# Optimization experiments

Hardware: AMD Instinct MI355X
Metric: run time of the kernel (lower is better)

The kernel has to match this reference:

```python
import jax, jax.numpy as jnp
import numpy as np

N_NODES = 5000
N_EDGES = 40000
NUM_ATOM_TYPES = 100
HID = 32            # multiplicity of 0e and 1o in irreps_hidden
EDGE_ATTR_DIM = 8
NUM_BOND_TYPES = 5
OUT_SCALARS = 2 * 6 + 1  # max_charge=6 -> 13x0e
CUTOFF = 5.0
SQRT3 = 1.7320508075688772


def _sh(edge_vec):
    # o3.SphericalHarmonics('1x0e + 1x1o', normalize=True, normalization='component')
    d = jnp.sqrt(jnp.sum(edge_vec * edge_vec, axis=-1) + 1e-12)
    n = edge_vec / d[:, None]
    sh0 = jnp.ones(edge_vec.shape[0], edge_vec.dtype)          # [E]
    sh1 = SQRT3 * n[:, (1, 2, 0)]                              # [E,3], e3nn (y,z,x) order
    return sh0, sh1, d


def _soft_one_hot(d):
    # e3nn.math.soft_one_hot_linspace(d, 0, cutoff, 8, basis='gaussian', cutoff=True)
    values = jnp.linspace(0.0, CUTOFF, EDGE_ATTR_DIM + 2)[1:-1]
    step = CUTOFF / (EDGE_ATTR_DIM + 1)
    diff = (d[:, None] - values[None, :]) / step
    return jnp.exp(-diff * diff) / 1.12


def _mlp(x, W0, b0, W1, b1):
    # ScalarMLP(in, out, hidden=[in], SiLU)
    return jax.nn.silu(x @ W0 + b0) @ W1 + b1


def _tp_init(s, sh0, sh1, w):
    # FCTP(32x0e, 1x0e+1x1o -> 32x0e+32x1o); paths: 0e*0e->0e, 0e*1o->1o
    E = s.shape[0]
    w1 = w[:, : HID * HID].reshape(E, HID, HID)
    w2 = w[:, HID * HID :].reshape(E, HID, HID)
    c = 1.0 / np.sqrt(HID)  # fan-in = 32 per output irrep
    out_s = c * jnp.einsum('eu,euw->ew', s * sh0[:, None], w1)
    out_v = c * jnp.einsum('eu,ei,euw->ewi', s, sh1, w2)
    return out_s, out_v


def _tp_hidden(s, v, sh0, sh1, w):
    # FCTP(32x0e+32x1o, 1x0e+1x1o -> 32x0e+32x1o)
    # path order: 0e*0e->0e, 0e*1o->1o, 1o*0e->1o, 1o*1o->0e
    E = s.shape[0]
    ws = w.reshape(E, 4, HID, HID)
    c = 1.0 / np.sqrt(2 * HID)  # fan-in = 64 per output irrep
    dot = jnp.einsum('eui,ei->eu', v, sh1) / SQRT3  # CG(1,1->0) = delta/sqrt(3)
    out_s = c * (jnp.einsum('eu,euw->ew', s * sh0[:, None], ws[:, 0]) +
                 jnp.einsum('eu,euw->ew', dot, ws[:, 3]))
    out_v = c * (jnp.einsum('eu,ei,euw->ewi', s, sh1, ws[:, 1]) +
                 jnp.einsum('eui,euw->ewi', v * sh0[:, None, None], ws[:, 2]))
    return out_s, out_v


def _edge_tp(s1, v1, s2, v2, sh0, sh1, w):
    # FCTP(64x0e+64x1o (concat of two hidden), 1x0e+1x1o -> 5x0e)
    # blocks in concat order: s_src, v_src, s_dst, v_dst
    E = s1.shape[0]
    ws = w.reshape(E, 4, HID, NUM_BOND_TYPES)
    c = 1.0 / np.sqrt(4 * HID)  # fan-in = 128
    d1 = jnp.einsum('eui,ei->eu', v1, sh1) / SQRT3
    d2 = jnp.einsum('eui,ei->eu', v2, sh1) / SQRT3
    return c * (jnp.einsum('eu,euw->ew', s1 * sh0[:, None], ws[:, 0]) +
                jnp.einsum('eu,euw->ew', d1, ws[:, 1]) +
                jnp.einsum('eu,euw->ew', s2 * sh0[:, None], ws[:, 2]) +
                jnp.einsum('eu,euw->ew', d2, ws[:, 3]))


def _scatter_mean(ms, mv, dst, n):
    cnt = jax.ops.segment_sum(jnp.ones(dst.shape[0], ms.dtype), dst, num_segments=n)
    cnt = jnp.maximum(cnt, 1.0)
    s = jax.ops.segment_sum(ms, dst, num_segments=n) / cnt[:, None]
    v = jax.ops.segment_sum(mv, dst, num_segments=n) / cnt[:, None, None]
    return s, v


def setup_inputs() -> dict:
    key = jax.random.key(0)
    ks = jax.random.split(key, 16)
    def w(k, shape, fan_in):
        return jax.random.normal(k, shape, dtype=jnp.float32) / np.sqrt(fan_in)
    inp = {}
    inp['coordinates'] = jax.random.normal(ks[0], (N_NODES, 3), dtype=jnp.float32) * 1.5
    inp['atom_types'] = jax.random.randint(ks[1], (N_NODES,), 0, NUM_ATOM_TYPES)
    inp['edge_index'] = jax.random.randint(ks[2], (2, N_EDGES), 0, N_NODES)
    inp['atom_embed'] = jax.random.normal(ks[3], (NUM_ATOM_TYPES, HID), dtype=jnp.float32)
    inp['ip_W0'] = w(ks[4], (EDGE_ATTR_DIM, EDGE_ATTR_DIM), EDGE_ATTR_DIM)
    inp['ip_b0'] = jnp.zeros((EDGE_ATTR_DIM,), jnp.float32)
    inp['ip_W1'] = w(ks[5], (EDGE_ATTR_DIM, 2 * HID * HID), EDGE_ATTR_DIM)
    inp['ip_b1'] = jnp.zeros((2 * HID * HID,), jnp.float32)
    inp['ly_W0'] = w(ks[6], (EDGE_ATTR_DIM, EDGE_ATTR_DIM), EDGE_ATTR_DIM)
    inp['ly_b0'] = jnp.zeros((EDGE_ATTR_DIM,), jnp.float32)
    inp['ly_W1'] = w(ks[7], (EDGE_ATTR_DIM, 4 * HID * HID), EDGE_ATTR_DIM)
    inp['ly_b1'] = jnp.zeros((4 * HID * HID,), jnp.float32)
    inp['ly_Ws'] = jax.random.normal(ks[8], (HID, HID), dtype=jnp.float32)
    inp['ly_Wv'] = jax.random.normal(ks[9], (HID, HID), dtype=jnp.float32)
    inp['et_W0'] = w(ks[10], (EDGE_ATTR_DIM, EDGE_ATTR_DIM), EDGE_ATTR_DIM)
    inp['et_b0'] = jnp.zeros((EDGE_ATTR_DIM,), jnp.float32)
    inp['et_W1'] = w(ks[11], (EDGE_ATTR_DIM, 4 * HID * NUM_BOND_TYPES), EDGE_ATTR_DIM)
    inp['et_b1'] = jnp.zeros((4 * HID * NUM_BOND_TYPES,), jnp.float32)
    inp['no_W1'] = jax.random.normal(ks[12], (HID, OUT_SCALARS), dtype=jnp.float32)
    inp['no_W2'] = jax.random.normal(ks[13], (OUT_SCALARS, OUT_SCALARS), dtype=jnp.float32)
    return inp


def reference(coordinates, atom_types, edge_index, atom_embed,
              ip_W0, ip_b0, ip_W1, ip_b1,
              ly_W0, ly_b0, ly_W1, ly_b1, ly_Ws, ly_Wv,
              et_W0, et_b0, et_W1, et_b1, no_W1, no_W2):
    n = coordinates.shape[0]
    src, dst = edge_index[0], edge_index[1]
    edge_vec = coordinates[dst] - coordinates[src]
    sh0, sh1, d = _sh(edge_vec)
    edge_attr = _soft_one_hot(d)                              # [E,8]
    # initial projector: Conv(32x0e -> 32x0e+32x1o)
    s0 = atom_embed[atom_types]                               # [N,32]
    w_ip = _mlp(edge_attr, ip_W0, ip_b0, ip_W1, ip_b1)        # [E,2048]
    ms, mv = _tp_init(s0[src], sh0, sh1, w_ip)
    s, v = _scatter_mean(ms, mv, dst, n)                      # [N,32],[N,32,3]
    # one LinearSelfInteraction(Conv) layer
    w_ly = _mlp(edge_attr, ly_W0, ly_b0, ly_W1, ly_b1)        # [E,4096]
    ms, mv = _tp_hidden(s[src], v[src], sh0, sh1, w_ly)
    cs, cv = _scatter_mean(ms, mv, dst, n)
    lc = 1.0 / np.sqrt(HID)  # e3nn o3.Linear normalization
    s = cs + lc * (s @ ly_Ws)
    v = cv + lc * jnp.einsum('eui,uw->ewi', v, ly_Wv)
    # edge output: FCTP([h_src, h_dst], edge_sh) with radial weights
    w_et = _mlp(edge_attr, et_W0, et_b0, et_W1, et_b1)        # [E,640]
    edge_out = _edge_tp(s[src], v[src], s[dst], v[dst], sh0, sh1, w_et)  # [E,5]
    # node output MLP on detached scalar channel (13x0e)
    sd = jax.lax.stop_gradient(s)
    h = jax.nn.silu(sd @ no_W1 / np.sqrt(HID))
    node_out = h @ no_W2 / np.sqrt(OUT_SCALARS)               # [N,13]
    return edge_out, node_out
```

## Files before the change

kernel.cpp:

```cpp
#include <hip/hip_runtime.h>

#define NN 5000
#define NE 40000
#define HB 320

typedef unsigned int u32;
typedef unsigned short u16;
typedef __fp16 h16x2 __attribute__((ext_vector_type(2)));
typedef _Float16 f16x8 __attribute__((ext_vector_type(8)));
typedef __attribute__((ext_vector_type(4))) float f32x4;

union AF { u32 u[4]; f16x8 v; uint4 q; };

__device__ __forceinline__ float siluf(float x) { return x / (1.f + __expf(-x)); }

__device__ __forceinline__ u32 f2bf_u(float f) {
  u32 x = __float_as_uint(f);
  return (x + 0x7FFFu + ((x >> 16) & 1u)) >> 16;
}
__device__ __forceinline__ u16 f2bf(float f) { return (u16)f2bf_u(f); }
__device__ __forceinline__ float bf2f(u16 v) { return __uint_as_float(((u32)v) << 16); }
__device__ __forceinline__ u32 packbf2(float lo, float hi) {
  return f2bf_u(lo) | (f2bf_u(hi) << 16);
}
__device__ __forceinline__ u32 pkh2(float a, float b) {
  union { h16x2 h; u32 u; } r;
  r.h = __builtin_amdgcn_cvt_pkrtz(a, b);
  return r.u;
}
__device__ __forceinline__ u16 f2h(float v) {
  _Float16 h = (_Float16)v;
  return *(u16*)&h;
}
__device__ __forceinline__ void unpack8(uint4 q, float* f) {
  f[0] = __uint_as_float(q.x << 16); f[1] = __uint_as_float(q.x & 0xFFFF0000u);
  f[2] = __uint_as_float(q.y << 16); f[3] = __uint_as_float(q.y & 0xFFFF0000u);
  f[4] = __uint_as_float(q.z << 16); f[5] = __uint_as_float(q.z & 0xFFFF0000u);
  f[6] = __uint_as_float(q.w << 16); f[7] = __uint_as_float(q.w & 0xFFFF0000u);
}
__device__ __forceinline__ float dot8f(const float* h, const float* w, float init) {
  float a = init;
#pragma unroll
  for (int k = 0; k < 8; k++) a = fmaf(h[k], w[k], a);
  return a;
}
__device__ __forceinline__ void mlp8(const float* ea, const float* __restrict__ W0,
                                     const float* __restrict__ b0, float* h) {
#pragma unroll
  for (int j = 0; j < 8; j++) {
    float a = b0[j];
#pragma unroll
    for (int i = 0; i < 8; i++) a += ea[i] * W0[i*8 + j];
    h[j] = siluf(a);
  }
}
__device__ __forceinline__ AF mkfrag(float hs, const float* s) {
  AF a;
  a.u[0] = pkh2(hs*s[0], hs*s[1]);
  a.u[1] = pkh2(hs*s[2], hs*s[3]);
  a.u[2] = pkh2(hs*s[4], hs*s[5]);
  a.u[3] = pkh2(hs*s[6], hs*s[7]);
  return a;
}

__global__ __launch_bounds__(256) void k_conv1g(
    const float* __restrict__ coords, const int* __restrict__ eidx,
    const float* __restrict__ emb, const int* __restrict__ atype,
    const float* __restrict__ ipW0, const float* __restrict__ ipb0,
    const float* __restrict__ lyW0, const float* __restrict__ lyb0,
    const float* __restrict__ etW0, const float* __restrict__ etb0,
    const float* __restrict__ W1, const float* __restrict__ b1,
    const float* __restrict__ lyW1, const float* __restrict__ lyb1,
    float* __restrict__ sh, float* __restrict__ h_ip,
    float* __restrict__ h_ly, float* __restrict__ h_et,
    int* __restrict__ cur, int* __restrict__ perm,
    u16* __restrict__ msg, u16* __restrict__ lyT) {
  if (blockIdx.x >= HB) {
    int b = blockIdx.x - HB;
    int h = b >> 3;
    int t0 = (b & 7)*2304 + threadIdx.x*9;
#pragma unroll
    for (int j = 0; j < 9; j++) {
      int t = t0 + j;
      int kch = t >> 9, rem = t & 511;
      int col = rem >> 3, kk = rem & 7;
      int k = kch*8 + kk;
      int basec = (h == 0) ? ((col >> 5)*1024 + (col & 31))
                           : ((col < 32) ? (2048 + col) : (3072 + (col - 32)));
      float v = (k < 256) ? lyW1[(k >> 5)*4096 + basec + (k & 31)*32]
                          : lyb1[basec + (k - 256)*32];
      lyT[h*18432 + t] = f2h(v);
    }
    return;
  }
  __shared__ __align__(16) u16 B2[36*64*8];
  {
    int col = threadIdx.x & 63, pth = col >> 5, w = col & 31;
    int k0 = (threadIdx.x >> 6) * 72;
    for (int k = k0; k < k0 + 72; k++) {
      float v = (k < 256) ? W1[(k >> 5)*2048 + pth*1024 + (k & 31)*32 + w]
                          : b1[pth*1024 + (k - 256)*32 + w];
      B2[((k >> 3)*64 + col)*8 + (k & 7)] = f2h(v);
    }
  }
  if (threadIdx.x < 128) {
    int idx = threadIdx.x;
    int w = (idx >> 4) & 3, j = idx >> 6, m = idx & 15;
    int tile = blockIdx.x*4 + w + j*(HB*4);
    if (tile*16 < NE) {
      int e = tile*16 + m;
      int s = eidx[e], d = eidx[NE + e];
      float vx = coords[d*3+0] - coords[s*3+0];
      float vy = coords[d*3+1] - coords[s*3+1];
      float vz = coords[d*3+2] - coords[s*3+2];
      float dist = sqrtf(vx*vx + vy*vy + vz*vz + 1e-12f);
      float inv = 1.f / dist;
      const float SQ3 = 1.7320508075688772f;
      sh[e*3+0] = SQ3 * vy * inv;
      sh[e*3+1] = SQ3 * vz * inv;
      sh[e*3+2] = SQ3 * vx * inv;
      float ea[8];
      const float step = 5.f / 9.f;
#pragma unroll
      for (int jj = 0; jj < 8; jj++) {
        float diff = (dist - step * (float)(jj+1)) * (9.f / 5.f);
        ea[jj] = __expf(-diff*diff) * (1.f / 1.12f);
      }
      float h[8];
      mlp8(ea, ipW0, ipb0, h);
#pragma unroll
      for (int jj = 0; jj < 8; jj++) h_ip[e*8+jj] = h[jj];
      mlp8(ea, lyW0, lyb0, h);
#pragma unroll
      for (int jj = 0; jj < 8; jj++) h_ly[e*8+jj] = h[jj];
      mlp8(ea, etW0, etb0, h);
#pragma unroll
      for (int jj = 0; jj < 8; jj++) h_et[e*8+jj] = h[jj];
      int* cp = &cur[d];
      atomicCAS(cp, (int)0xAAAAAAAA, 0);
      int t = atomicAdd(cp, 1);
      if (t < 64) perm[d*64 + t] = e;
    }
  }
  __syncthreads();
  int lane = threadIdx.x & 63;
  int m = lane & 15, q = lane >> 4, wid = threadIdx.x >> 6;
  const float cs = 0.17677669529663687f;
  for (int tile = blockIdx.x*4 + wid; tile*16 < NE; tile += HB*4) {
    int e = tile*16 + m;
    int srow = atype[eidx[e]];
    float4 sA = *(const float4*)&emb[srow*32 + q*8];
    float4 sB = *(const float4*)&emb[srow*32 + q*8 + 4];
    float4 hA = *(const float4*)&h_ip[e*8];
    float4 hB = *(const float4*)&h_ip[e*8 + 4];
    float sf[8] = {sA.x,sA.y,sA.z,sA.w,sB.x,sB.y,sB.z,sB.w};
    float hf[8] = {hA.x,hA.y,hA.z,hA.w,hB.x,hB.y,hB.z,hB.w};
    f32x4 acc0 = {0.f,0.f,0.f,0.f}, acc1 = acc0, acc2 = acc0, acc3 = acc0;
#pragma unroll
    for (int ks = 0; ks < 9; ks++) {
      float hs = (ks < 8) ? hf[ks] : 1.f;
      AF a = mkfrag(hs, sf);
      int c2 = (ks*4 + q)*64;
      AF b0, b1f, b2, b3;
      b0.q  = *(const uint4*)&B2[(c2 +  0 + m)*8];
      b1f.q = *(const uint4*)&B2[(c2 + 16 + m)*8];
      b2.q  = *(const uint4*)&B2[(c2 + 32 + m)*8];
      b3.q  = *(const uint4*)&B2[(c2 + 48 + m)*8];
      acc0 = __builtin_amdgcn_mfma_f32_16x16x32_f16(a.v, b0.v,  acc0, 0, 0, 0);
      acc1 = __builtin_amdgcn_mfma_f32_16x16x32_f16(a.v, b1f.v, acc1, 0, 0, 0);
      acc2 = __builtin_amdgcn_mfma_f32_16x16x32_f16(a.v, b2.v,  acc2, 0, 0, 0);
      acc3 = __builtin_amdgcn_mfma_f32_16x16x32_f16(a.v, b3.v,  acc3, 0, 0, 0);
    }
#pragma unroll
    for (int r = 0; r < 4; r++) {
      int et = tile*16 + q*4 + r;
      u16* mp = msg + (size_t)et*128;
      mp[m]      = f2bf(cs*acc0[r]);
      mp[16 + m] = f2bf(cs*acc1[r]);
      float s0v = sh[et*3+0], s1v = sh[et*3+1], s2v = sh[et*3+2];
      float m0 = cs*acc2[r], m1 = cs*acc3[r];
      mp[32 +      m] = f2bf(m0*s0v);
      mp[64 +      m] = f2bf(m0*s1v);
      mp[96 +      m] = f2bf(m0*s2v);
      mp[32 + 16 + m] = f2bf(m1*s0v);
      mp[64 + 16 + m] = f2bf(m1*s1v);
      mp[96 + 16 + m] = f2bf(m1*s2v);
    }
  }
}

__global__ __launch_bounds__(256) void k_conv2(
    const float* __restrict__ hE, const float* __restrict__ sh,
    const float* __restrict__ s1, const float* __restrict__ v1soa,
    const int* __restrict__ eidx, const u16* __restrict__ lyT,
    u16* __restrict__ msgA, u16* __restrict__ msgB) {
  __shared__ __align__(16) u16 B2[36*64*8];
  const bool scalarHalf = blockIdx.x < HB;
  int blk = scalarHalf ? blockIdx.x : blockIdx.x - HB;
  {
    const uint4* src4 = (const uint4*)(lyT + (scalarHalf ? 0 : 18432));
    uint4* dst4 = (uint4*)B2;
    for (int t = threadIdx.x; t < 2304; t += 256) dst4[t] = src4[t];
  }
  __syncthreads();
  int lane = threadIdx.x & 63;
  int m = lane & 15, q = lane >> 4, wid = threadIdx.x >> 6;
  const float c = 0.125f;
  for (int tile = blk*4 + wid; tile*16 < NE; tile += HB*4) {
    int e = tile*16 + m;
    int srcn = eidx[e];
    float4 hA = *(const float4*)&hE[e*8];
    float4 hB = *(const float4*)&hE[e*8 + 4];
    float hf[8] = {hA.x,hA.y,hA.z,hA.w,hB.x,hB.y,hB.z,hB.w};

    if (scalarHalf) {
      float4 sA = *(const float4*)&s1[srcn*32 + q*8];
      float4 sB = *(const float4*)&s1[srcn*32 + q*8 + 4];
      float sf[8] = {sA.x,sA.y,sA.z,sA.w,sB.x,sB.y,sB.z,sB.w};
      f32x4 acc0 = {0.f,0.f,0.f,0.f}, acc1 = acc0, acc2 = acc0, acc3 = acc0;
#pragma unroll
      for (int ks = 0; ks < 9; ks++) {
        float hs = (ks < 8) ? hf[ks] : 1.f;
        AF a = mkfrag(hs, sf);
        int c2 = (ks*4 + q)*64;
        AF b0, b1f, b2, b3;
        b0.q  = *(const uint4*)&B2[(c2 +  0 + m)*8];
        b1f.q = *(const uint4*)&B2[(c2 + 16 + m)*8];
        b2.q  = *(const uint4*)&B2[(c2 + 32 + m)*8];
        b3.q  = *(const uint4*)&B2[(c2 + 48 + m)*8];
        acc0 = __builtin_amdgcn_mfma_f32_16x16x32_f16(a.v, b0.v,  acc0, 0, 0, 0);
        acc1 = __builtin_amdgcn_mfma_f32_16x16x32_f16(a.v, b1f.v, acc1, 0, 0, 0);
        acc2 = __builtin_amdgcn_mfma_f32_16x16x32_f16(a.v, b2.v,  acc2, 0, 0, 0);
        acc3 = __builtin_amdgcn_mfma_f32_16x16x32_f16(a.v, b3.v,  acc3, 0, 0, 0);
      }
#pragma unroll
      for (int r = 0; r < 4; r++) {
        int et = tile*16 + q*4 + r;
        u16* mp = msgA + (size_t)et*128;
        mp[m]      = f2bf(c*acc0[r]);
        mp[16 + m] = f2bf(c*acc1[r]);
        float s0v = sh[et*3+0], s1v = sh[et*3+1], s2v = sh[et*3+2];
        float m0 = c*acc2[r], m1 = c*acc3[r];
        mp[32 +      m] = f2bf(m0*s0v);
        mp[64 +      m] = f2bf(m0*s1v);
        mp[96 +      m] = f2bf(m0*s2v);
        mp[32 + 16 + m] = f2bf(m1*s0v);
        mp[64 + 16 + m] = f2bf(m1*s1v);
        mp[96 + 16 + m] = f2bf(m1*s2v);
      }
    } else {
      const float is3 = 0.5773502691896258f;
      float vf[3][8];
#pragma unroll
      for (int i = 0; i < 3; i++) {
        float4 aa = *(const float4*)&v1soa[i*160000 + srcn*32 + q*8];
        float4 bb = *(const float4*)&v1soa[i*160000 + srcn*32 + q*8 + 4];
        vf[i][0]=aa.x; vf[i][1]=aa.y; vf[i][2]=aa.z; vf[i][3]=aa.w;
        vf[i][4]=bb.x; vf[i][5]=bb.y; vf[i][6]=bb.z; vf[i][7]=bb.w;
      }
      float es0 = sh[e*3+0], es1 = sh[e*3+1], es2 = sh[e*3+2];
      float df[8];
#pragma unroll
      for (int j = 0; j < 8; j++)
        df[j] = (vf[0][j]*es0 + vf[1][j]*es1 + vf[2][j]*es2) * is3;
      f32x4 z = {0.f,0.f,0.f,0.f};
      f32x4 aV00 = z, aV01 = z, aV10 = z, aV11 = z, aV20 = z, aV21 = z, aD0 = z, aD1 = z;
#pragma unroll
      for (int ks = 0; ks < 9; ks++) {
        float hs = (ks < 8) ? hf[ks] : 1.f;
        int c2 = (ks*4 + q)*64;
        AF b0, b1f, b2, b3;
        b0.q  = *(const uint4*)&B2[(c2 +  0 + m)*8];
        b1f.q = *(const uint4*)&B2[(c2 + 16 + m)*8];
        b2.q  = *(const uint4*)&B2[(c2 + 32 + m)*8];
        b3.q  = *(const uint4*)&B2[(c2 + 48 + m)*8];
        AF a0 = mkfrag(hs, vf[0]);
        AF a1 = mkfrag(hs, vf[1]);
        AF a2 = mkfrag(hs, vf[2]);
        AF ad = mkfrag(hs, df);
        aV00 = __builtin_amdgcn_mfma_f32_16x16x32_f16(a0.v, b0.v,  aV00, 0, 0, 0);
        aV01 = __builtin_amdgcn_mfma_f32_16x16x32_f16(a0.v, b1f.v, aV01, 0, 0, 0);
        aV10 = __builtin_amdgcn_mfma_f32_16x16x32_f16(a1.v, b0.v,  aV10, 0, 0, 0);
        aV11 = __builtin_amdgcn_mfma_f32_16x16x32_f16(a1.v, b1f.v, aV11, 0, 0, 0);
        aV20 = __builtin_amdgcn_mfma_f32_16x16x32_f16(a2.v, b0.v,  aV20, 0, 0, 0);
        aV21 = __builtin_amdgcn_mfma_f32_16x16x32_f16(a2.v, b1f.v, aV21, 0, 0, 0);
        aD0  = __builtin_amdgcn_mfma_f32_16x16x32_f16(ad.v, b2.v,  aD0,  0, 0, 0);
        aD1  = __builtin_amdgcn_mfma_f32_16x16x32_f16(ad.v, b3.v,  aD1,  0, 0, 0);
      }
#pragma unroll
      for (int r = 0; r < 4; r++) {
        int et = tile*16 + q*4 + r;
        u16* mp = msgB + (size_t)et*128;
        mp[m]      = f2bf(c*aD0[r]);
        mp[16 + m] = f2bf(c*aD1[r]);
        mp[32 +      m] = f2bf(c*aV00[r]);
        mp[32 + 16 + m] = f2bf(c*aV01[r]);
        mp[64 +      m] = f2bf(c*aV10[r]);
        mp[64 + 16 + m] = f2bf(c*aV11[r]);
        mp[96 +      m] = f2bf(c*aV20[r]);
        mp[96 + 16 + m] = f2bf(c*aV21[r]);
      }
    }
  }
}

__global__ __launch_bounds__(256) void k_gather1(
    const u16* __restrict__ msg, const int* __restrict__ perm,
    const int* __restrict__ cur, float* __restrict__ s1,
    float* __restrict__ v1soa) {
  __shared__ int pe[2][64];
  int ln = threadIdx.x >> 7, c = threadIdx.x & 127;
  int n = blockIdx.x*2 + ln;
  int deg = min(cur[n], 64);
  if (c < 64) pe[ln][c] = perm[n*64 + c];
  __syncthreads();
  float acc = 0.f;
  for (int j = 0; j < deg; j++)
    acc += bf2f(msg[(size_t)pe[ln][j]*128 + c]);
  acc /= (float)max(deg, 1);
  if (c < 32) s1[n*32 + c] = acc;
  else { int i = (c-32) >> 5, w = (c-32) & 31; v1soa[i*160000 + n*32 + w] = acc; }
}

__global__ __launch_bounds__(256) void k_gather2(
    const u16* __restrict__ msgA, const u16* __restrict__ msgB,
    const int* __restrict__ perm, const int* __restrict__ cur,
    const float* __restrict__ s1, const float* __restrict__ v1soa,
    const float* __restrict__ Ws, const float* __restrict__ Wv,
    const float* __restrict__ noW1, const float* __restrict__ noW2,
    float* __restrict__ s2, float* __restrict__ v2, float* __restrict__ outN) {
  __shared__ int pe[2][64];
  __shared__ float sb[2][32];
  __shared__ float hb[2][13];
  int ln = threadIdx.x >> 7, c = threadIdx.x & 127;
  int n = blockIdx.x*2 + ln;
  int deg = min(cur[n], 64);
  if (c < 64) pe[ln][c] = perm[n*64 + c];
  __syncthreads();
  float acc = 0.f;
  for (int j = 0; j < deg; j++) {
    int e = pe[ln][j];
    acc += bf2f(msgA[(size_t)e*128 + c]) + bf2f(msgB[(size_t)e*128 + c]);
  }
  acc /= (float)max(deg, 1);
  const float lc = 0.17677669529663687f;
  if (c < 32) {
    float ss = 0.f;
#pragma unroll 8
    for (int u = 0; u < 32; u++) ss += s1[n*32 + u] * Ws[u*32 + c];
    float val = acc + lc*ss;
    s2[n*32 + c] = val;
    sb[ln][c] = val;
  } else {
    int i = (c-32) >> 5, w = (c-32) & 31;
    float sv = 0.f;
#pragma unroll 8
    for (int u = 0; u < 32; u++) sv += v1soa[i*160000 + n*32 + u] * Wv[u*32 + w];
    v2[n*96 + w*3 + i] = acc + lc*sv;
  }
  __syncthreads();
  const float i32 = 0.17677669529663687f;
  if (c < 13) {
    float a = 0.f;
#pragma unroll 8
    for (int u = 0; u < 32; u++) a += sb[ln][u] * noW1[u*13 + c];
    hb[ln][c] = siluf(a * i32);
  }
  __syncthreads();
  const float i13 = 0.2773500981126146f;
  if (c < 13) {
    float a = 0.f;
#pragma unroll
    for (int j = 0; j < 13; j++) a += hb[ln][j] * noW2[j*13 + c];
    outN[n*13 + c] = a * i13;
  }
}

__global__ __launch_bounds__(256) void k_e3(
    const float* __restrict__ hE, const float* __restrict__ sh,
    const float* __restrict__ s2, const float* __restrict__ v2,
    const int* __restrict__ eidx,
    const float* __restrict__ W1, const float* __restrict__ b1,
    float* __restrict__ out) {
  __shared__ uint4 WQ[640];
  __shared__ float BQ[640];
  for (int t = threadIdx.x; t < 640; t += 256) {
    int u = t & 31, pw = t >> 5, p2 = pw / 5, w = pw - p2*5;
    int col = p2*160 + u*5 + w;
    const float* s = W1 + col;
    uint4 q;
    q.x = packbf2(s[0],      s[640]);
    q.y = packbf2(s[1280],   s[1920]);
    q.z = packbf2(s[2560],   s[3200]);
    q.w = packbf2(s[3840],   s[4480]);
    WQ[t] = q;
    BQ[t] = b1[col];
  }
  __syncthreads();
  const int g = threadIdx.x >> 5, tw = threadIdx.x & 31;
  const float c = 0.08838834764831845f;
  const float is3 = 0.5773502691896258f;
  for (int p = blockIdx.x*8 + g; p*2 < NE; p += gridDim.x*8) {
    int e0 = p*2, e1 = e0 + 1;
    float h0[8], h1[8];
    {
      float4 qa = *(const float4*)&hE[e0*8];
      float4 qb = *(const float4*)&hE[e0*8+4];
      h0[0]=qa.x; h0[1]=qa.y; h0[2]=qa.z; h0[3]=qa.w;
      h0[4]=qb.x; h0[5]=qb.y; h0[6]=qb.z; h0[7]=qb.w;
      float4 qc = *(const float4*)&hE[e1*8];
      float4 qd = *(const float4*)&hE[e1*8+4];
      h1[0]=qc.x; h1[1]=qc.y; h1[2]=qc.z; h1[3]=qc.w;
      h1[4]=qd.x; h1[5]=qd.y; h1[6]=qd.z; h1[7]=qd.w;
    }
    int sA = eidx[e0], dA = eidx[NE+e0];
    int sB = eidx[e1], dB = eidx[NE+e1];
    float sa0 = sh[e0*3+0], sa1 = sh[e0*3+1], sa2 = sh[e0*3+2];
    float sb0 = sh[e1*3+0], sb1 = sh[e1*3+1], sb2 = sh[e1*3+2];
    float c00 = s2[sA*32 + tw];
    float c01 = (v2[sA*96+tw*3+0]*sa0 + v2[sA*96+tw*3+1]*sa1 + v2[sA*96+tw*3+2]*sa2) * is3;
    float c02 = s2[dA*32 + tw];
    float c03 = (v2[dA*96+tw*3+0]*sa0 + v2[dA*96+tw*3+1]*sa1 + v2[dA*96+tw*3+2]*sa2) * is3;
    float c10 = s2[sB*32 + tw];
    float c11 = (v2[sB*96+tw*3+0]*sb0 + v2[sB*96+tw*3+1]*sb1 + v2[sB*96+tw*3+2]*sb2) * is3;
    float c12 = s2[dB*32 + tw];
    float c13 = (v2[dB*96+tw*3+0]*sb0 + v2[dB*96+tw*3+1]*sb1 + v2[dB*96+tw*3+2]*sb2) * is3;
    float part0[5] = {0,0,0,0,0};
    float part1[5] = {0,0,0,0,0};
#pragma unroll
    for (int pp = 0; pp < 4; pp++) {
      float cp0 = (pp==0) ? c00 : (pp==1) ? c01 : (pp==2) ? c02 : c03;
      float cp1 = (pp==0) ? c10 : (pp==1) ? c11 : (pp==2) ? c12 : c13;
#pragma unroll
      for (int w = 0; w < 5; w++) {
        int idx = (pp*5 + w)*32 + tw;
        float f[8];
        unpack8(WQ[idx], f);
        float bv = BQ[idx];
        part0[w] = fmaf(cp0, dot8f(h0, f, bv), part0[w]);
        part1[w] = fmaf(cp1, dot8f(h1, f, bv), part1[w]);
      }
    }
#pragma unroll
    for (int off = 16; off > 0; off >>= 1)
#pragma unroll
      for (int w = 0; w < 5; w++) {
        part0[w] += __shfl_xor(part0[w], off, 32);
        part1[w] += __shfl_xor(part1[w], off, 32);
      }
    float outv = 0.f;
#pragma unroll
    for (int w = 0; w < 5; w++) {
      if (tw == w)     outv = part0[w];
      if (tw == 5 + w) outv = part1[w];
    }
    if (tw < 10) out[e0*5 + tw] = c * outv;
  }
}

extern "C" void kernel_launch(void* const* d_in, const int* in_sizes, int n_in,
                              void* d_out, int out_size, void* d_ws, size_t ws_size,
                              hipStream_t stream) {
  (void)in_sizes; (void)n_in; (void)out_size; (void)ws_size;
  const float* coords = (const float*)d_in[0];
  const int*   atype  = (const int*)d_in[1];
  const int*   eidx   = (const int*)d_in[2];
  const float* emb    = (const float*)d_in[3];
  const float* ipW0 = (const float*)d_in[4];
  const float* ipb0 = (const float*)d_in[5];
  const float* ipW1 = (const float*)d_in[6];
  const float* ipb1 = (const float*)d_in[7];
  const float* lyW0 = (const float*)d_in[8];
  const float* lyb0 = (const float*)d_in[9];
  const float* lyW1 = (const float*)d_in[10];
  const float* lyb1 = (const float*)d_in[11];
  const float* lyWs = (const float*)d_in[12];
  const float* lyWv = (const float*)d_in[13];
  const float* etW0 = (const float*)d_in[14];
  const float* etb0 = (const float*)d_in[15];
  const float* etW1 = (const float*)d_in[16];
  const float* etb1 = (const float*)d_in[17];
  const float* noW1 = (const float*)d_in[18];
  const float* noW2 = (const float*)d_in[19];

  float* ws = (float*)d_ws;
  float* sh    = ws;
  float* h_ip  = ws + 120000;
  float* h_ly  = ws + 440000;
  float* h_et  = ws + 760000;
  float* s1    = ws + 1240000;
  float* v1soa = ws + 1400000;
  float* s2    = ws + 1880000;
  float* v2    = ws + 2040000;
  int*   cur   = (int*)(ws + 2520000);
  int*   perm  = (int*)(ws + 2525000);
  u16*   msgA  = (u16*)(ws + 2845000);
  u16*   msgB  = (u16*)(ws + 5405000);
  u16*   lyT   = (u16*)(ws + 7965000);

  float* outE = (float*)d_out;
  float* outN = (float*)d_out + NE*5;

  k_conv1g<<<HB + 16, 256, 0, stream>>>(coords, eidx, emb, atype,
                                        ipW0, ipb0, lyW0, lyb0, etW0, etb0,
                                        ipW1, ipb1, lyW1, lyb1,
                                        sh, h_ip, h_ly, h_et, cur, perm, msgA, lyT);
  k_gather1<<<NN/2, 256, 0, stream>>>(msgA, perm, cur, s1, v1soa);
  k_conv2<<<2*HB, 256, 0, stream>>>(h_ly, sh, s1, v1soa, eidx, lyT, msgA, msgB);
  k_gather2<<<NN/2, 256, 0, stream>>>(msgA, msgB, perm, cur, s1, v1soa,
                                      lyWs, lyWv, noW1, noW2, s2, v2, outN);
  k_e3<<<1024, 256, 0, stream>>>(h_et, sh, s2, v2, eidx, etW1, etb1, outE);
}
```

Measured before the change: 170.0 us.

## Fuse all five stage kernels into one cooperative persistent kernel with grid syncs

Replaces the five separate launches (conv1, gather1, conv2, gather2, edge output) with one cooperative kernel that moves between stages using grid.sync. The goal is to remove the launch gaps and tail effects between the small kernels. The grid size is capped by occupancy and MAXGRID, so each stage now runs as a grid-stride loop over fewer blocks than the original per-kernel launch sizes. The gathers are also reworked to give one wavefront per node, reading the per-node edge list through shuffles. The costs are grid-barrier overhead, less parallelism in the stages that previously used large grids, and a tighter register budget under launch_bounds(256,2).

```diff
diff --git a/kernel.cpp b/kernel.cpp
--- a/kernel.cpp
+++ b/kernel.cpp
@@ -1,8 +1,11 @@
 #include <hip/hip_runtime.h>
+#include <hip/hip_cooperative_groups.h>
+
+namespace cg = cooperative_groups;
 
 #define NN 5000
 #define NE 40000
-#define HB 320
+#define MAXGRID 512
 
 typedef unsigned int u32;
 typedef unsigned short u16;
@@ -63,22 +66,38 @@
   return a;
 }
 
-__global__ __launch_bounds__(256) void k_conv1g(
-    const float* __restrict__ coords, const int* __restrict__ eidx,
-    const float* __restrict__ emb, const int* __restrict__ atype,
-    const float* __restrict__ ipW0, const float* __restrict__ ipb0,
-    const float* __restrict__ lyW0, const float* __restrict__ lyb0,
-    const float* __restrict__ etW0, const float* __restrict__ etb0,
-    const float* __restrict__ W1, const float* __restrict__ b1,
-    const float* __restrict__ lyW1, const float* __restrict__ lyb1,
-    float* __restrict__ sh, float* __restrict__ h_ip,
-    float* __restrict__ h_ly, float* __restrict__ h_et,
-    int* __restrict__ cur, int* __restrict__ perm,
-    u16* __restrict__ msg, u16* __restrict__ lyT) {
-  if (blockIdx.x >= HB) {
-    int b = blockIdx.x - HB;
+struct Par {
+  const float* coords; const int* atype; const int* eidx; const float* emb;
+  const float* ipW0; const float* ipb0; const float* ipW1; const float* ipb1;
+  const float* lyW0; const float* lyb0; const float* lyW1; const float* lyb1;
+  const float* lyWs; const float* lyWv;
+  const float* etW0; const float* etb0; const float* etW1; const float* etb1;
+  const float* noW1; const float* noW2;
+  float* sh; float* h_ip; float* h_ly; float* h_et;
+  float* s1; float* v1soa; float* s2; float* v2;
+  int* cur; int* perm; u16* msgA; u16* msgB; u16* lyT;
+  float* outE; float* outN;
+};
+
+union SMem {
+  u16 B2[18432];
+  struct { uint4 WQ[640]; float BQ[640]; } e;
+};
+
+__global__ __launch_bounds__(256, 2) void k_all(Par par) {
+  __shared__ SMem sm;
+  cg::grid_group grid = cg::this_grid();
+  const int tid = threadIdx.x;
+  const int bid = blockIdx.x;
+  const int lane = tid & 63;
+  const int m = lane & 15, q = lane >> 4, wid = tid >> 6;
+  const int ngrid = (int)gridDim.x;
+  const int ncb = ngrid - 16;
+
+  if (bid >= ncb) {
+    int b = bid - ncb;
     int h = b >> 3;
-    int t0 = (b & 7)*2304 + threadIdx.x*9;
+    int t0 = (b & 7)*2304 + tid*9;
 #pragma unroll
     for (int j = 0; j < 9; j++) {
       int t = t0 + j;
@@ -87,136 +106,70 @@
       int k = kch*8 + kk;
       int basec = (h == 0) ? ((col >> 5)*1024 + (col & 31))
                            : ((col < 32) ? (2048 + col) : (3072 + (col - 32)));
-      float v = (k < 256) ? lyW1[(k >> 5)*4096 + basec + (k & 31)*32]
-                          : lyb1[basec + (k - 256)*32];
-      lyT[h*18432 + t] = f2h(v);
-    }
-    return;
-  }
-  __shared__ __align__(16) u16 B2[36*64*8];
-  {
-    int col = threadIdx.x & 63, pth = col >> 5, w = col & 31;
-    int k0 = (threadIdx.x >> 6) * 72;
-    for (int k = k0; k < k0 + 72; k++) {
-      float v = (k < 256) ? W1[(k >> 5)*2048 + pth*1024 + (k & 31)*32 + w]
-                          : b1[pth*1024 + (k - 256)*32 + w];
-      B2[((k >> 3)*64 + col)*8 + (k & 7)] = f2h(v);
-    }
-  }
-  if (threadIdx.x < 128) {
-    int idx = threadIdx.x;
-    int w = (idx >> 4) & 3, j = idx >> 6, m = idx & 15;
-    int tile = blockIdx.x*4 + w + j*(HB*4);
-    if (tile*16 < NE) {
+      float v = (k < 256) ? par.lyW1[(k >> 5)*4096 + basec + (k & 31)*32]
+                          : par.lyb1[basec + (k - 256)*32];
+      par.lyT[h*18432 + t] = f2h(v);
+    }
+  } else {
+    {
+      int col = tid & 63, pth = col >> 5, w = col & 31;
+      int k0 = (tid >> 6) * 72;
+      for (int k = k0; k < k0 + 72; k++) {
+        float v = (k < 256) ? par.ipW1[(k >> 5)*2048 + pth*1024 + (k & 31)*32 + w]
+                            : par.ipb1[pth*1024 + (k - 256)*32 + w];
+        sm.B2[((k >> 3)*64 + col)*8 + (k & 7)] = f2h(v);
+      }
+    }
+    if (tid < 128) {
+      int w = (tid >> 4) & 3, mm = tid & 15, jj0 = tid >> 6;
+      for (int it = jj0; ; it += 2) {
+        int tile = bid*4 + w + it*(ncb*4);
+        if (tile*16 >= NE) break;
+        int e = tile*16 + mm;
+        int s = par.eidx[e], d = par.eidx[NE + e];
+        float vx = par.coords[d*3+0] - par.coords[s*3+0];
+        float vy = par.coords[d*3+1] - par.coords[s*3+1];
+        float vz = par.coords[d*3+2] - par.coords[s*3+2];
+        float dist = sqrtf(vx*vx + vy*vy + vz*vz + 1e-12f);
+        float inv = 1.f / dist;
+        const float SQ3 = 1.7320508075688772f;
+        par.sh[e*3+0] = SQ3 * vy * inv;
+        par.sh[e*3+1] = SQ3 * vz * inv;
+        par.sh[e*3+2] = SQ3 * vx * inv;
+        float ea[8];
+        const float step = 5.f / 9.f;
+#pragma unroll
+        for (int jj = 0; jj < 8; jj++) {
+          float diff = (dist - step * (float)(jj+1)) * (9.f / 5.f);
+          ea[jj] = __expf(-diff*diff) * (1.f / 1.12f);
+        }
+        float h[8];
+        mlp8(ea, par.ipW0, par.ipb0, h);
+#pragma unroll
+        for (int jj = 0; jj < 8; jj++) par.h_ip[e*8+jj] = h[jj];
+        mlp8(ea, par.lyW0, par.lyb0, h);
+#pragma unroll
+        for (int jj = 0; jj < 8; jj++) par.h_ly[e*8+jj] = h[jj];
+        mlp8(ea, par.etW0, par.etb0, h);
+#pragma unroll
+        for (int jj = 0; jj < 8; jj++) par.h_et[e*8+jj] = h[jj];
+        int* cp = &par.cur[d];
+        atomicCAS(cp, (int)0xAAAAAAAA, 0);
+        int t = atomicAdd(cp, 1);
+        if (t < 64) par.perm[d*64 + t] = e;
+      }
+    }
+    __syncthreads();
+    const float cs = 0.17677669529663687f;
+    for (int tile = bid*4 + wid; tile*16 < NE; tile += ncb*4) {
       int e = tile*16 + m;
-      int s = eidx[e], d = eidx[NE + e];
-      float vx = coords[d*3+0] - coords[s*3+0];
-      float vy = coords[d*3+1] - coords[s*3+1];
-      float vz = coords[d*3+2] - coords[s*3+2];
-      float dist = sqrtf(vx*vx + vy*vy + vz*vz + 1e-12f);
-      float inv = 1.f / dist;
-      const float SQ3 = 1.7320508075688772f;
-      sh[e*3+0] = SQ3 * vy * inv;
-      sh[e*3+1] = SQ3 * vz * inv;
-      sh[e*3+2] = SQ3 * vx * inv;
-      float ea[8];
-      const float step = 5.f / 9.f;
-#pragma unroll
-      for (int jj = 0; jj < 8; jj++) {
-        float diff = (dist - step * (float)(jj+1)) * (9.f / 5.f);
-        ea[jj] = __expf(-diff*diff) * (1.f / 1.12f);
-      }
-      float h[8];
-      mlp8(ea, ipW0, ipb0, h);
-#pragma unroll
-      for (int jj = 0; jj < 8; jj++) h_ip[e*8+jj] = h[jj];
-      mlp8(ea, lyW0, lyb0, h);
-#pragma unroll
-      for (int jj = 0; jj < 8; jj++) h_ly[e*8+jj] = h[jj];
-      mlp8(ea, etW0, etb0, h);
-#pragma unroll
-      for (int jj = 0; jj < 8; jj++) h_et[e*8+jj] = h[jj];
-      int* cp = &cur[d];
-      atomicCAS(cp, (int)0xAAAAAAAA, 0);
-      int t = atomicAdd(cp, 1);
-      if (t < 64) perm[d*64 + t] = e;
-    }
-  }
-  __syncthreads();
-  int lane = threadIdx.x & 63;
-  int m = lane & 15, q = lane >> 4, wid = threadIdx.x >> 6;
-  const float cs = 0.17677669529663687f;
-  for (int tile = blockIdx.x*4 + wid; tile*16 < NE; tile += HB*4) {
-    int e = tile*16 + m;
-    int srow = atype[eidx[e]];
-    float4 sA = *(const float4*)&emb[srow*32 + q*8];
-    float4 sB = *(const float4*)&emb[srow*32 + q*8 + 4];
-    float4 hA = *(const float4*)&h_ip[e*8];
-    float4 hB = *(const float4*)&h_ip[e*8 + 4];
-    float sf[8] = {sA.x,sA.y,sA.z,sA.w,sB.x,sB.y,sB.z,sB.w};
-    float hf[8] = {hA.x,hA.y,hA.z,hA.w,hB.x,hB.y,hB.z,hB.w};
-    f32x4 acc0 = {0.f,0.f,0.f,0.f}, acc1 = acc0, acc2 = acc0, acc3 = acc0;
-#pragma unroll
-    for (int ks = 0; ks < 9; ks++) {
-      float hs = (ks < 8) ? hf[ks] : 1.f;
-      AF a = mkfrag(hs, sf);
-      int c2 = (ks*4 + q)*64;
-      AF b0, b1f, b2, b3;
-      b0.q  = *(const uint4*)&B2[(c2 +  0 + m)*8];
-      b1f.q = *(const uint4*)&B2[(c2 + 16 + m)*8];
-      b2.q  = *(const uint4*)&B2[(c2 + 32 + m)*8];
-      b3.q  = *(const uint4*)&B2[(c2 + 48 + m)*8];
-      acc0 = __builtin_amdgcn_mfma_f32_16x16x32_f16(a.v, b0.v,  acc0, 0, 0, 0);
-      acc1 = __builtin_amdgcn_mfma_f32_16x16x32_f16(a.v, b1f.v, acc1, 0, 0, 0);
-      acc2 = __builtin_amdgcn_mfma_f32_16x16x32_f16(a.v, b2.v,  acc2, 0, 0, 0);
-      acc3 = __builtin_amdgcn_mfma_f32_16x16x32_f16(a.v, b3.v,  acc3, 0, 0, 0);
-    }
-#pragma unroll
-    for (int r = 0; r < 4; r++) {
-      int et = tile*16 + q*4 + r;
-      u16* mp = msg + (size_t)et*128;
-      mp[m]      = f2bf(cs*acc0[r]);
-      mp[16 + m] = f2bf(cs*acc1[r]);
-      float s0v = sh[et*3+0], s1v = sh[et*3+1], s2v = sh[et*3+2];
-      float m0 = cs*acc2[r], m1 = cs*acc3[r];
-      mp[32 +      m] = f2bf(m0*s0v);
-      mp[64 +      m] = f2bf(m0*s1v);
-      mp[96 +      m] = f2bf(m0*s2v);
-      mp[32 + 16 + m] = f2bf(m1*s0v);
-      mp[64 + 16 + m] = f2bf(m1*s1v);
-      mp[96 + 16 + m] = f2bf(m1*s2v);
-    }
-  }
-}
-
-__global__ __launch_bounds__(256) void k_conv2(
-    const float* __restrict__ hE, const float* __restrict__ sh,
-    const float* __restrict__ s1, const float* __restrict__ v1soa,
-    const int* __restrict__ eidx, const u16* __restrict__ lyT,
-    u16* __restrict__ msgA, u16* __restrict__ msgB) {
-  __shared__ __align__(16) u16 B2[36*64*8];
-  const bool scalarHalf = blockIdx.x < HB;
-  int blk = scalarHalf ? blockIdx.x : blockIdx.x - HB;
-  {
-    const uint4* src4 = (const uint4*)(lyT + (scalarHalf ? 0 : 18432));
-    uint4* dst4 = (uint4*)B2;
-    for (int t = threadIdx.x; t < 2304; t += 256) dst4[t] = src4[t];
-  }
-  __syncthreads();
-  int lane = threadIdx.x & 63;
-  int m = lane & 15, q = lane >> 4, wid = threadIdx.x >> 6;
-  const float c = 0.125f;
-  for (int tile = blk*4 + wid; tile*16 < NE; tile += HB*4) {
-    int e = tile*16 + m;
-    int srcn = eidx[e];
-    float4 hA = *(const float4*)&hE[e*8];
-    float4 hB = *(const float4*)&hE[e*8 + 4];
-    float hf[8] = {hA.x,hA.y,hA.z,hA.w,hB.x,hB.y,hB.z,hB.w};
-
-    if (scalarHalf) {
-      float4 sA = *(const float4*)&s1[srcn*32 + q*8];
-      float4 sB = *(const float4*)&s1[srcn*32 + q*8 + 4];
+      int srow = par.atype[par.eidx[e]];
+      float4 sA = *(const float4*)&par.emb[srow*32 + q*8];
+      float4 sB = *(const float4*)&par.emb[srow*32 + q*8 + 4];
+      float4 hA = *(const float4*)&par.h_ip[e*8];
+      float4 hB = *(const float4*)&par.h_ip[e*8 + 4];
       float sf[8] = {sA.x,sA.y,sA.z,sA.w,sB.x,sB.y,sB.z,sB.w};
+      float hf[8] = {hA.x,hA.y,hA.z,hA.w,hB.x,hB.y,hB.z,hB.w};
       f32x4 acc0 = {0.f,0.f,0.f,0.f}, acc1 = acc0, acc2 = acc0, acc3 = acc0;
 #pragma unroll
       for (int ks = 0; ks < 9; ks++) {
@@ -224,10 +177,10 @@
         AF a = mkfrag(hs, sf);
         int c2 = (ks*4 + q)*64;
         AF b0, b1f, b2, b3;
-        b0.q  = *(const uint4*)&B2[(c2 +  0 + m)*8];
-        b1f.q = *(const uint4*)&B2[(c2 + 16 + m)*8];
-        b2.q  = *(const uint4*)&B2[(c2 + 32 + m)*8];
-        b3.q  = *(const uint4*)&B2[(c2 + 48 + m)*8];
+        b0.q  = *(const uint4*)&sm.B2[(c2 +  0 + m)*8];
+        b1f.q = *(const uint4*)&sm.B2[(c2 + 16 + m)*8];
+        b2.q  = *(const uint4*)&sm.B2[(c2 + 32 + m)*8];
+        b3.q  = *(const uint4*)&sm.B2[(c2 + 48 + m)*8];
         acc0 = __builtin_amdgcn_mfma_f32_16x16x32_f16(a.v, b0.v,  acc0, 0, 0, 0);
         acc1 = __builtin_amdgcn_mfma_f32_16x16x32_f16(a.v, b1f.v, acc1, 0, 0, 0);
         acc2 = __builtin_amdgcn_mfma_f32_16x16x32_f16(a.v, b2.v,  acc2, 0, 0, 0);
@@ -236,11 +189,11 @@
 #pragma unroll
       for (int r = 0; r < 4; r++) {
         int et = tile*16 + q*4 + r;
-        u16* mp = msgA + (size_t)et*128;
-        mp[m]      = f2bf(c*acc0[r]);
-        mp[16 + m] = f2bf(c*acc1[r]);
-        float s0v = sh[et*3+0], s1v = sh[et*3+1], s2v = sh[et*3+2];
-        float m0 = c*acc2[r], m1 = c*acc3[r];
+        u16* mp = par.msgA + (size_t)et*128;
+        mp[m]      = f2bf(cs*acc0[r]);
+        mp[16 + m] = f2bf(cs*acc1[r]);
+        float s0v = par.sh[et*3+0], s1v = par.sh[et*3+1], s2v = par.sh[et*3+2];
+        float m0 = cs*acc2[r], m1 = cs*acc3[r];
         mp[32 +      m] = f2bf(m0*s0v);
         mp[64 +      m] = f2bf(m0*s1v);
         mp[96 +      m] = f2bf(m0*s2v);
@@ -248,213 +201,268 @@
         mp[64 + 16 + m] = f2bf(m1*s1v);
         mp[96 + 16 + m] = f2bf(m1*s2v);
       }
-    } else {
-      const float is3 = 0.5773502691896258f;
-      float vf[3][8];
-#pragma unroll
-      for (int i = 0; i < 3; i++) {
-        float4 aa = *(const float4*)&v1soa[i*160000 + srcn*32 + q*8];
-        float4 bb = *(const float4*)&v1soa[i*160000 + srcn*32 + q*8 + 4];
-        vf[i][0]=aa.x; vf[i][1]=aa.y; vf[i][2]=aa.z; vf[i][3]=aa.w;
-        vf[i][4]=bb.x; vf[i][5]=bb.y; vf[i][6]=bb.z; vf[i][7]=bb.w;
-      }
-      float es0 = sh[e*3+0], es1 = sh[e*3+1], es2 = sh[e*3+2];
-      float df[8];
-#pragma unroll
-      for (int j = 0; j < 8; j++)
-        df[j] = (vf[0][j]*es0 + vf[1][j]*es1 + vf[2][j]*es2) * is3;
-      f32x4 z = {0.f,0.f,0.f,0.f};
-      f32x4 aV00 = z, aV01 = z, aV10 = z, aV11 = z, aV20 = z, aV21 = z, aD0 = z, aD1 = z;
-#pragma unroll
-      for (int ks = 0; ks < 9; ks++) {
-        float hs = (ks < 8) ? hf[ks] : 1.f;
-        int c2 = (ks*4 + q)*64;
-        AF b0, b1f, b2, b3;
-        b0.q  = *(const uint4*)&B2[(c2 +  0 + m)*8];
-        b1f.q = *(const uint4*)&B2[(c2 + 16 + m)*8];
-        b2.q  = *(const uint4*)&B2[(c2 + 32 + m)*8];
-        b3.q  = *(const uint4*)&B2[(c2 + 48 + m)*8];
-        AF a0 = mkfrag(hs, vf[0]);
-        AF a1 = mkfrag(hs, vf[1]);
-        AF a2 = mkfrag(hs, vf[2]);
-        AF ad = mkfrag(hs, df);
-        aV00 = __builtin_amdgcn_mfma_f32_16x16x32_f16(a0.v, b0.v,  aV00, 0, 0, 0);
-        aV01 = __builtin_amdgcn_mfma_f32_16x16x32_f16(a0.v, b1f.v, aV01, 0, 0, 0);
-        aV10 = __builtin_amdgcn_mfma_f32_16x16x32_f16(a1.v, b0.v,  aV10, 0, 0, 0);
-        aV11 = __builtin_amdgcn_mfma_f32_16x16x32_f16(a1.v, b1f.v, aV11, 0, 0, 0);
-        aV20 = __builtin_amdgcn_mfma_f32_16x16x32_f16(a2.v, b0.v,  aV20, 0, 0, 0);
-        aV21 = __builtin_amdgcn_mfma_f32_16x16x32_f16(a2.v, b1f.v, aV21, 0, 0, 0);
-        aD0  = __builtin_amdgcn_mfma_f32_16x16x32_f16(ad.v, b2.v,  aD0,  0, 0, 0);
-        aD1  = __builtin_amdgcn_mfma_f32_16x16x32_f16(ad.v, b3.v,  aD1,  0, 0, 0);
-      }
-#pragma unroll
-      for (int r = 0; r < 4; r++) {
-        int et = tile*16 + q*4 + r;
-        u16* mp = msgB + (size_t)et*128;
-        mp[m]      = f2bf(c*aD0[r]);
-        mp[16 + m] = f2bf(c*aD1[r]);
-        mp[32 +      m] = f2bf(c*aV00[r]);
-        mp[32 + 16 + m] = f2bf(c*aV01[r]);
-        mp[64 +      m] = f2bf(c*aV10[r]);
-        mp[64 + 16 + m] = f2bf(c*aV11[r]);
-        mp[96 +      m] = f2bf(c*aV20[r]);
-        mp[96 + 16 + m] = f2bf(c*aV21[r]);
-      }
-    }
-  }
-}
-
-__global__ __launch_bounds__(256) void k_gather1(
-    const u16* __restrict__ msg, const int* __restrict__ perm,
-    const int* __restrict__ cur, float* __restrict__ s1,
-    float* __restrict__ v1soa) {
-  __shared__ int pe[2][64];
-  int ln = threadIdx.x >> 7, c = threadIdx.x & 127;
-  int n = blockIdx.x*2 + ln;
-  int deg = min(cur[n], 64);
-  if (c < 64) pe[ln][c] = perm[n*64 + c];
-  __syncthreads();
-  float acc = 0.f;
-  for (int j = 0; j < deg; j++)
-    acc += bf2f(msg[(size_t)pe[ln][j]*128 + c]);
-  acc /= (float)max(deg, 1);
-  if (c < 32) s1[n*32 + c] = acc;
-  else { int i = (c-32) >> 5, w = (c-32) & 31; v1soa[i*160000 + n*32 + w] = acc; }
-}
-
-__global__ __launch_bounds__(256) void k_gather2(
-    const u16* __restrict__ msgA, const u16* __restrict__ msgB,
-    const int* __restrict__ perm, const int* __restrict__ cur,
-    const float* __restrict__ s1, const float* __restrict__ v1soa,
-    const float* __restrict__ Ws, const float* __restrict__ Wv,
-    const float* __restrict__ noW1, const float* __restrict__ noW2,
-    float* __restrict__ s2, float* __restrict__ v2, float* __restrict__ outN) {
-  __shared__ int pe[2][64];
-  __shared__ float sb[2][32];
-  __shared__ float hb[2][13];
-  int ln = threadIdx.x >> 7, c = threadIdx.x & 127;
-  int n = blockIdx.x*2 + ln;
-  int deg = min(cur[n], 64);
-  if (c < 64) pe[ln][c] = perm[n*64 + c];
-  __syncthreads();
-  float acc = 0.f;
-  for (int j = 0; j < deg; j++) {
-    int e = pe[ln][j];
-    acc += bf2f(msgA[(size_t)e*128 + c]) + bf2f(msgB[(size_t)e*128 + c]);
-  }
-  acc /= (float)max(deg, 1);
-  const float lc = 0.17677669529663687f;
-  if (c < 32) {
-    float ss = 0.f;
+    }
+  }
+  __threadfence();
+  grid.sync();
+
+  {
+    int wg = (bid << 2) | wid;
+    for (int n = wg; n < NN; n += ngrid*4) {
+      int deg = min(par.cur[n], 64);
+      int pv = par.perm[n*64 + lane];
+      float a0 = 0.f, a1 = 0.f;
+      for (int j = 0; j < deg; j++) {
+        int e = __shfl(pv, j, 64);
+        size_t off = (size_t)e*128 + lane;
+        a0 += bf2f(par.msgA[off]);
+        a1 += bf2f(par.msgA[off + 64]);
+      }
+      float inv = 1.f / (float)max(deg, 1);
+      a0 *= inv; a1 *= inv;
+      if (lane < 32) par.s1[n*32 + lane] = a0;
+      else           par.v1soa[n*32 + (lane - 32)] = a0;
+      int i = 1 + (lane >> 5), w = lane & 31;
+      par.v1soa[i*160000 + n*32 + w] = a1;
+    }
+  }
+  __threadfence();
+  grid.sync();
+
+  {
+    const int half = ngrid >> 1;
+    const bool scalarHalf = bid < half;
+    int blk = scalarHalf ? bid : bid - half;
+    const uint4* src4 = (const uint4*)(par.lyT + (scalarHalf ? 0 : 18432));
+    uint4* dst4 = (uint4*)sm.B2;
+    for (int t = tid; t < 2304; t += 256) dst4[t] = src4[t];
+    __syncthreads();
+    const float c = 0.125f;
+    for (int tile = blk*4 + wid; tile*16 < NE; tile += half*4) {
+      int e = tile*16 + m;
+      int srcn = par.eidx[e];
+      float4 hA = *(const float4*)&par.h_ly[e*8];
+      float4 hB = *(const float4*)&par.h_ly[e*8 + 4];
+      float hf[8] = {hA.x,hA.y,hA.z,hA.w,hB.x,hB.y,hB.z,hB.w};
+
+      if (scalarHalf) {
+        float4 sA = *(const float4*)&par.s1[srcn*32 + q*8];
+        float4 sB = *(const float4*)&par.s1[srcn*32 + q*8 + 4];
+        float sf[8] = {sA.x,sA.y,sA.z,sA.w,sB.x,sB.y,sB.z,sB.w};
+        f32x4 acc0 = {0.f,0.f,0.f,0.f}, acc1 = acc0, acc2 = acc0, acc3 = acc0;
+#pragma unroll
+        for (int ks = 0; ks < 9; ks++) {
+          float hs = (ks < 8) ? hf[ks] : 1.f;
+          AF a = mkfrag(hs, sf);
+          int c2 = (ks*4 + q)*64;
+          AF b0, b1f, b2, b3;
+          b0.q  = *(const uint4*)&sm.B2[(c2 +  0 + m)*8];
+          b1f.q = *(const uint4*)&sm.B2[(c2 + 16 + m)*8];
+          b2.q  = *(const uint4*)&sm.B2[(c2 + 32 + m)*8];
+          b3.q  = *(const uint4*)&sm.B2[(c2 + 48 + m)*8];
+          acc0 = __builtin_amdgcn_mfma_f32_16x16x32_f16(a.v, b0.v,  acc0, 0, 0, 0);
+          acc1 = __builtin_amdgcn_mfma_f32_16x16x32_f16(a.v, b1f.v, acc1, 0, 0, 0);
+          acc2 = __builtin_amdgcn_mfma_f32_16x16x32_f16(a.v, b2.v,  acc2, 0, 0, 0);
+          acc3 = __builtin_amdgcn_mfma_f32_16x16x32_f16(a.v, b3.v,  acc3, 0, 0, 0);
+        }
+#pragma unroll
+        for (int r = 0; r < 4; r++) {
+          int et = tile*16 + q*4 + r;
+          u16* mp = par.msgA + (size_t)et*128;
+          mp[m]      = f2bf(c*acc0[r]);
+          mp[16 + m] = f2bf(c*acc1[r]);
+          float s0v = par.sh[et*3+0], s1v = par.sh[et*3+1], s2v = par.sh[et*3+2];
+          float m0 = c*acc2[r], m1 = c*acc3[r];
+          mp[32 +      m] = f2bf(m0*s0v);
+          mp[64 +      m] = f2bf(m0*s1v);
+          mp[96 +      m] = f2bf(m0*s2v);
+          mp[32 + 16 + m] = f2bf(m1*s0v);
+          mp[64 + 16 + m] = f2bf(m1*s1v);
+          mp[96 + 16 + m] = f2bf(m1*s2v);
+        }
+      } else {
+        const float is3 = 0.5773502691896258f;
+        float vf[3][8];
+#pragma unroll
+        for (int i = 0; i < 3; i++) {
+          float4 aa = *(const float4*)&par.v1soa[i*160000 + srcn*32 + q*8];
+          float4 bb = *(const float4*)&par.v1soa[i*160000 + srcn*32 + q*8 + 4];
+          vf[i][0]=aa.x; vf[i][1]=aa.y; vf[i][2]=aa.z; vf[i][3]=aa.w;
+          vf[i][4]=bb.x; vf[i][5]=bb.y; vf[i][6]=bb.z; vf[i][7]=bb.w;
+        }
+        float es0 = par.sh[e*3+0], es1 = par.sh[e*3+1], es2 = par.sh[e*3+2];
+        float df[8];
+#pragma unroll
+        for (int j = 0; j < 8; j++)
+          df[j] = (vf[0][j]*es0 + vf[1][j]*es1 + vf[2][j]*es2) * is3;
+        f32x4 z = {0.f,0.f,0.f,0.f};
+        f32x4 aV00 = z, aV01 = z, aV10 = z, aV11 = z, aV20 = z, aV21 = z, aD0 = z, aD1 = z;
+#pragma unroll
+        for (int ks = 0; ks < 9; ks++) {
+          float hs = (ks < 8) ? hf[ks] : 1.f;
+          int c2 = (ks*4 + q)*64;
+          AF b0, b1f, b2, b3;
+          b0.q  = *(const uint4*)&sm.B2[(c2 +  0 + m)*8];
+          b1f.q = *(const uint4*)&sm.B2[(c2 + 16 + m)*8];
+          b2.q  = *(const uint4*)&sm.B2[(c2 + 32 + m)*8];
+          b3.q  = *(const uint4*)&sm.B2[(c2 + 48 + m)*8];
+          AF a0 = mkfrag(hs, vf[0]);
+          AF a1 = mkfrag(hs, vf[1]);
+          AF a2 = mkfrag(hs, vf[2]);
+          AF ad = mkfrag(hs, df);
+          aV00 = __builtin_amdgcn_mfma_f32_16x16x32_f16(a0.v, b0.v,  aV00, 0, 0, 0);
+          aV01 = __builtin_amdgcn_mfma_f32_16x16x32_f16(a0.v, b1f.v, aV01, 0, 0, 0);
+          aV10 = __builtin_amdgcn_mfma_f32_16x16x32_f16(a1.v, b0.v,  aV10, 0, 0, 0);
+          aV11 = __builtin_amdgcn_mfma_f32_16x16x32_f16(a1.v, b1f.v, aV11, 0, 0, 0);
+          aV20 = __builtin_amdgcn_mfma_f32_16x16x32_f16(a2.v, b0.v,  aV20, 0, 0, 0);
+          aV21 = __builtin_amdgcn_mfma_f32_16x16x32_f16(a2.v, b1f.v, aV21, 0, 0, 0);
+          aD0  = __builtin_amdgcn_mfma_f32_16x16x32_f16(ad.v, b2.v,  aD0,  0, 0, 0);
+          aD1  = __builtin_amdgcn_mfma_f32_16x16x32_f16(ad.v, b3.v,  aD1,  0, 0, 0);
+        }
+#pragma unroll
+        for (int r = 0; r < 4; r++) {
+          int et = tile*16 + q*4 + r;
+          u16* mp = par.msgB + (size_t)et*128;
+          mp[m]      = f2bf(c*aD0[r]);
+          mp[16 + m] = f2bf(c*aD1[r]);
+          mp[32 +      m] = f2bf(c*aV00[r]);
+          mp[32 + 16 + m] = f2bf(c*aV01[r]);
+          mp[64 +      m] = f2bf(c*aV10[r]);
+          mp[64 + 16 + m] = f2bf(c*aV11[r]);
+          mp[96 +      m] = f2bf(c*aV20[r]);
+          mp[96 + 16 + m] = f2bf(c*aV21[r]);
+        }
+      }
+    }
+  }
+  __threadfence();
+  grid.sync();
+
+  {
+    const float lc = 0.17677669529663687f;
+    const float i32c = 0.17677669529663687f;
+    const float i13c = 0.2773500981126146f;
+    int wg = (bid << 2) | wid;
+    int c13 = (lane < 13) ? lane : 0;
+    for (int n = wg; n < NN; n += ngrid*4) {
+      int deg = min(par.cur[n], 64);
+      int pv = par.perm[n*64 + lane];
+      float a0 = 0.f, a1 = 0.f;
+      for (int j = 0; j < deg; j++) {
+        int e = __shfl(pv, j, 64);
+        size_t off = (size_t)e*128 + lane;
+        a0 += bf2f(par.msgA[off])      + bf2f(par.msgB[off]);
+        a1 += bf2f(par.msgA[off + 64]) + bf2f(par.msgB[off + 64]);
+      }
+      float inv = 1.f / (float)max(deg, 1);
+      a0 *= inv; a1 *= inv;
+      float s2v = 0.f;
+      if (lane < 32) {
+        float ss = 0.f;
 #pragma unroll 8
-    for (int u = 0; u < 32; u++) ss += s1[n*32 + u] * Ws[u*32 + c];
-    float val = acc + lc*ss;
-    s2[n*32 + c] = val;
-    sb[ln][c] = val;
-  } else {
-    int i = (c-32) >> 5, w = (c-32) & 31;
-    float sv = 0.f;
+        for (int u = 0; u < 32; u++) ss += par.s1[n*32 + u] * par.lyWs[u*32 + lane];
+        s2v = a0 + lc*ss;
+        par.s2[n*32 + lane] = s2v;
+      } else {
+        int w0 = lane & 31;
+        float sv = 0.f;
 #pragma unroll 8
-    for (int u = 0; u < 32; u++) sv += v1soa[i*160000 + n*32 + u] * Wv[u*32 + w];
-    v2[n*96 + w*3 + i] = acc + lc*sv;
-  }
-  __syncthreads();
-  const float i32 = 0.17677669529663687f;
-  if (c < 13) {
-    float a = 0.f;
+        for (int u = 0; u < 32; u++) sv += par.v1soa[n*32 + u] * par.lyWv[u*32 + w0];
+        par.v2[n*96 + w0*3 + 0] = a0 + lc*sv;
+      }
+      {
+        int i = 1 + (lane >> 5), w0 = lane & 31;
+        float sv = 0.f;
 #pragma unroll 8
-    for (int u = 0; u < 32; u++) a += sb[ln][u] * noW1[u*13 + c];
-    hb[ln][c] = siluf(a * i32);
-  }
-  __syncthreads();
-  const float i13 = 0.2773500981126146f;
-  if (c < 13) {
-    float a = 0.f;
-#pragma unroll
-    for (int j = 0; j < 13; j++) a += hb[ln][j] * noW2[j*13 + c];
-    outN[n*13 + c] = a * i13;
-  }
-}
-
-__global__ __launch_bounds__(256) void k_e3(
-    const float* __restrict__ hE, const float* __restrict__ sh,
-    const float* __restrict__ s2, const float* __restrict__ v2,
-    const int* __restrict__ eidx,
-    const float* __restrict__ W1, const float* __restrict__ b1,
-    float* __restrict__ out) {
-  __shared__ uint4 WQ[640];
-  __shared__ float BQ[640];
-  for (int t = threadIdx.x; t < 640; t += 256) {
-    int u = t & 31, pw = t >> 5, p2 = pw / 5, w = pw - p2*5;
-    int col = p2*160 + u*5 + w;
-    const float* s = W1 + col;
-    uint4 q;
-    q.x = packbf2(s[0],      s[640]);
-    q.y = packbf2(s[1280],   s[1920]);
-    q.z = packbf2(s[2560],   s[3200]);
-    q.w = packbf2(s[3840],   s[4480]);
-    WQ[t] = q;
-    BQ[t] = b1[col];
-  }
-  __syncthreads();
-  const int g = threadIdx.x >> 5, tw = threadIdx.x & 31;
-  const float c = 0.08838834764831845f;
-  const float is3 = 0.5773502691896258f;
-  for (int p = blockIdx.x*8 + g; p*2 < NE; p += gridDim.x*8) {
-    int e0 = p*2, e1 = e0 + 1;
-    float h0[8], h1[8];
-    {
-      float4 qa = *(const float4*)&hE[e0*8];
-      float4 qb = *(const float4*)&hE[e0*8+4];
-      h0[0]=qa.x; h0[1]=qa.y; h0[2]=qa.z; h0[3]=qa.w;
-      h0[4]=qb.x; h0[5]=qb.y; h0[6]=qb.z; h0[7]=qb.w;
-      float4 qc = *(const float4*)&hE[e1*8];
-      float4 qd = *(const float4*)&hE[e1*8+4];
-      h1[0]=qc.x; h1[1]=qc.y; h1[2]=qc.z; h1[3]=qc.w;
-      h1[4]=qd.x; h1[5]=qd.y; h1[6]=qd.z; h1[7]=qd.w;
-    }
-    int sA = eidx[e0], dA = eidx[NE+e0];
-    int sB = eidx[e1], dB = eidx[NE+e1];
-    float sa0 = sh[e0*3+0], sa1 = sh[e0*3+1], sa2 = sh[e0*3+2];
-    float sb0 = sh[e1*3+0], sb1 = sh[e1*3+1], sb2 = sh[e1*3+2];
-    float c00 = s2[sA*32 + tw];
-    float c01 = (v2[sA*96+tw*3+0]*sa0 + v2[sA*96+tw*3+1]*sa1 + v2[sA*96+tw*3+2]*sa2) * is3;
-    float c02 = s2[dA*32 + tw];
-    float c03 = (v2[dA*96+tw*3+0]*sa0 + v2[dA*96+tw*3+1]*sa1 + v2[dA*96+tw*3+2]*sa2) * is3;
-    float c10 = s2[sB*32 + tw];
-    float c11 = (v2[sB*96+tw*3+0]*sb0 + v2[sB*96+tw*3+1]*sb1 + v2[sB*96+tw*3+2]*sb2) * is3;
-    float c12 = s2[dB*32 + tw];
-    float c13 = (v2[dB*96+tw*3+0]*sb0 + v2[dB*96+tw*3+1]*sb1 + v2[dB*96+tw*3+2]*sb2) * is3;
-    float part0[5] = {0,0,0,0,0};
-    float part1[5] = {0,0,0,0,0};
-#pragma unroll
-    for (int pp = 0; pp < 4; pp++) {
-      float cp0 = (pp==0) ? c00 : (pp==1) ? c01 : (pp==2) ? c02 : c03;
-      float cp1 = (pp==0) ? c10 : (pp==1) ? c11 : (pp==2) ? c12 : c13;
+        for (int u = 0; u < 32; u++) sv += par.v1soa[i*160000 + n*32 + u] * par.lyWv[u*32 + w0];
+        par.v2[n*96 + w0*3 + i] = a1 + lc*sv;
+      }
+      float a = 0.f;
+#pragma unroll 8
+      for (int u = 0; u < 32; u++) a += __shfl(s2v, u, 64) * par.noW1[u*13 + c13];
+      float hv = siluf(a * i32c);
+      float o = 0.f;
+#pragma unroll
+      for (int j = 0; j < 13; j++) o += __shfl(hv, j, 64) * par.noW2[j*13 + c13];
+      if (lane < 13) par.outN[n*13 + lane] = o * i13c;
+    }
+  }
+  __threadfence();
+  grid.sync();
+
+  {
+    for (int t = tid; t < 640; t += 256) {
+      int u = t & 31, pw = t >> 5, p2 = pw / 5, w = pw - p2*5;
+      int col = p2*160 + u*5 + w;
+      const float* s = par.etW1 + col;
+      uint4 qq;
+      qq.x = packbf2(s[0],      s[640]);
+      qq.y = packbf2(s[1280],   s[1920]);
+      qq.z = packbf2(s[2560],   s[3200]);
+      qq.w = packbf2(s[3840],   s[4480]);
+      sm.e.WQ[t] = qq;
+      sm.e.BQ[t] = par.etb1[col];
+    }
+    __syncthreads();
+    const int g = tid >> 5, tw = tid & 31;
+    const float ce = 0.08838834764831845f;
+    const float is3 = 0.5773502691896258f;
+    for (int pr = bid*8 + g; pr*2 < NE; pr += ngrid*8) {
+      int e0 = pr*2, e1 = e0 + 1;
+      float h0[8], h1[8];
+      {
+        float4 qa = *(const float4*)&par.h_et[e0*8];
+        float4 qb = *(const float4*)&par.h_et[e0*8+4];
+        h0[0]=qa.x; h0[1]=qa.y; h0[2]=qa.z; h0[3]=qa.w;
+        h0[4]=qb.x; h0[5]=qb.y; h0[6]=qb.z; h0[7]=qb.w;
+        float4 qc = *(const float4*)&par.h_et[e1*8];
+        float4 qd = *(const float4*)&par.h_et[e1*8+4];
+        h1[0]=qc.x; h1[1]=qc.y; h1[2]=qc.z; h1[3]=qc.w;
+        h1[4]=qd.x; h1[5]=qd.y; h1[6]=qd.z; h1[7]=qd.w;
+      }
+      int sA = par.eidx[e0], dA = par.eidx[NE+e0];
+      int sB = par.eidx[e1], dB = par.eidx[NE+e1];
+      float sa0 = par.sh[e0*3+0], sa1 = par.sh[e0*3+1], sa2 = par.sh[e0*3+2];
+      float sb0 = par.sh[e1*3+0], sb1 = par.sh[e1*3+1], sb2 = par.sh[e1*3+2];
+      float c00 = par.s2[sA*32 + tw];
+      float c01 = (par.v2[sA*96+tw*3+0]*sa0 + par.v2[sA*96+tw*3+1]*sa1 + par.v2[sA*96+tw*3+2]*sa2) * is3;
+      float c02 = par.s2[dA*32 + tw];
+      float c03 = (par.v2[dA*96+tw*3+0]*sa0 + par.v2[dA*96+tw*3+1]*sa1 + par.v2[dA*96+tw*3+2]*sa2) * is3;
+      float c10 = par.s2[sB*32 + tw];
+      float c11 = (par.v2[sB*96+tw*3+0]*sb0 + par.v2[sB*96+tw*3+1]*sb1 + par.v2[sB*96+tw*3+2]*sb2) * is3;
+      float c12 = par.s2[dB*32 + tw];
+      float c13 = (par.v2[dB*96+tw*3+0]*sb0 + par.v2[dB*96+tw*3+1]*sb1 + par.v2[dB*96+tw*3+2]*sb2) * is3;
+      float part0[5] = {0,0,0,0,0};
+      float part1[5] = {0,0,0,0,0};
+#pragma unroll
+      for (int pp = 0; pp < 4; pp++) {
+        float cp0 = (pp==0) ? c00 : (pp==1) ? c01 : (pp==2) ? c02 : c03;
+        float cp1 = (pp==0) ? c10 : (pp==1) ? c11 : (pp==2) ? c12 : c13;
+#pragma unroll
+        for (int w = 0; w < 5; w++) {
+          int idx = (pp*5 + w)*32 + tw;
+          float f[8];
+          unpack8(sm.e.WQ[idx], f);
+          float bv = sm.e.BQ[idx];
+          part0[w] = fmaf(cp0, dot8f(h0, f, bv), part0[w]);
+          part1[w] = fmaf(cp1, dot8f(h1, f, bv), part1[w]);
+        }
+      }
+#pragma unroll
+      for (int off = 16; off > 0; off >>= 1)
+#pragma unroll
+        for (int w = 0; w < 5; w++) {
+          part0[w] += __shfl_xor(part0[w], off, 32);
+          part1[w] += __shfl_xor(part1[w], off, 32);
+        }
+      float outv = 0.f;
 #pragma unroll
       for (int w = 0; w < 5; w++) {
-        int idx = (pp*5 + w)*32 + tw;
-        float f[8];
-        unpack8(WQ[idx], f);
-        float bv = BQ[idx];
-        part0[w] = fmaf(cp0, dot8f(h0, f, bv), part0[w]);
-        part1[w] = fmaf(cp1, dot8f(h1, f, bv), part1[w]);
-      }
-    }
-#pragma unroll
-    for (int off = 16; off > 0; off >>= 1)
-#pragma unroll
-      for (int w = 0; w < 5; w++) {
-        part0[w] += __shfl_xor(part0[w], off, 32);
-        part1[w] += __shfl_xor(part1[w], off, 32);
-      }
-    float outv = 0.f;
-#pragma unroll
-    for (int w = 0; w < 5; w++) {
-      if (tw == w)     outv = part0[w];
-      if (tw == 5 + w) outv = part1[w];
-    }
-    if (tw < 10) out[e0*5 + tw] = c * outv;
+        if (tw == w)     outv = part0[w];
+        if (tw == 5 + w) outv = part1[w];
+      }
+      if (tw < 10) par.outE[e0*5 + tw] = ce * outv;
+    }
   }
 }
 
@@ -462,52 +470,57 @@
                               void* d_out, int out_size, void* d_ws, size_t ws_size,
                               hipStream_t stream) {
   (void)in_sizes; (void)n_in; (void)out_size; (void)ws_size;
-  const float* coords = (const float*)d_in[0];
-  const int*   atype  = (const int*)d_in[1];
-  const int*   eidx   = (const int*)d_in[2];
-  const float* emb    = (const float*)d_in[3];
-  const float* ipW0 = (const float*)d_in[4];
-  const float* ipb0 = (const float*)d_in[5];
-  const float* ipW1 = (const float*)d_in[6];
-  const float* ipb1 = (const float*)d_in[7];
-  const float* lyW0 = (const float*)d_in[8];
-  const float* lyb0 = (const float*)d_in[9];
-  const float* lyW1 = (const float*)d_in[10];
-  const float* lyb1 = (const float*)d_in[11];
-  const float* lyWs = (const float*)d_in[12];
-  const float* lyWv = (const float*)d_in[13];
-  const float* etW0 = (const float*)d_in[14];
-  const float* etb0 = (const float*)d_in[15];
-  const float* etW1 = (const float*)d_in[16];
-  const float* etb1 = (const float*)d_in[17];
-  const float* noW1 = (const float*)d_in[18];
-  const float* noW2 = (const float*)d_in[19];
-
   float* ws = (float*)d_ws;
-  float* sh    = ws;
-  float* h_ip  = ws + 120000;
-  float* h_ly  = ws + 440000;
-  float* h_et  = ws + 760000;
-  float* s1    = ws + 1240000;
-  float* v1soa = ws + 1400000;
-  float* s2    = ws + 1880000;
-  float* v2    = ws + 2040000;
-  int*   cur   = (int*)(ws + 2520000);
-  int*   perm  = (int*)(ws + 2525000);
-  u16*   msgA  = (u16*)(ws + 2845000);
-  u16*   msgB  = (u16*)(ws + 5405000);
-  u16*   lyT   = (u16*)(ws + 7965000);
-
-  float* outE = (float*)d_out;
-  float* outN = (float*)d_out + NE*5;
-
-  k_conv1g<<<HB + 16, 256, 0, stream>>>(coords, eidx, emb, atype,
-                                        ipW0, ipb0, lyW0, lyb0, etW0, etb0,
-                                        ipW1, ipb1, lyW1, lyb1,
-                                        sh, h_ip, h_ly, h_et, cur, perm, msgA, lyT);
-  k_gather1<<<NN/2, 256, 0, stream>>>(msgA, perm, cur, s1, v1soa);
-  k_conv2<<<2*HB, 256, 0, stream>>>(h_ly, sh, s1, v1soa, eidx, lyT, msgA, msgB);
-  k_gather2<<<NN/2, 256, 0, stream>>>(msgA, msgB, perm, cur, s1, v1soa,
-                                      lyWs, lyWv, noW1, noW2, s2, v2, outN);
-  k_e3<<<1024, 256, 0, stream>>>(h_et, sh, s2, v2, eidx, etW1, etb1, outE);
-}
+  Par par;
+  par.coords = (const float*)d_in[0];
+  par.atype  = (const int*)d_in[1];
+  par.eidx   = (const int*)d_in[2];
+  par.emb    = (const float*)d_in[3];
+  par.ipW0 = (const float*)d_in[4];
+  par.ipb0 = (const float*)d_in[5];
+  par.ipW1 = (const float*)d_in[6];
+  par.ipb1 = (const float*)d_in[7];
+  par.lyW0 = (const float*)d_in[8];
+  par.lyb0 = (const float*)d_in[9];
+  par.lyW1 = (const float*)d_in[10];
+  par.lyb1 = (const float*)d_in[11];
+  par.lyWs = (const float*)d_in[12];
+  par.lyWv = (const float*)d_in[13];
+  par.etW0 = (const float*)d_in[14];
+  par.etb0 = (const float*)d_in[15];
+  par.etW1 = (const float*)d_in[16];
+  par.etb1 = (const float*)d_in[17];
+  par.noW1 = (const float*)d_in[18];
+  par.noW2 = (const float*)d_in[19];
+  par.sh    = ws;
+  par.h_ip  = ws + 120000;
+  par.h_ly  = ws + 440000;
+  par.h_et  = ws + 760000;
+  par.s1    = ws + 1240000;
+  par.v1soa = ws + 1400000;
+  par.s2    = ws + 1880000;
+  par.v2    = ws + 2040000;
+  par.cur   = (int*)(ws + 2520000);
+  par.perm  = (int*)(ws + 2525000);
+  par.msgA  = (u16*)(ws + 2845000);
+  par.msgB  = (u16*)(ws + 5405000);
+  par.lyT   = (u16*)(ws + 7965000);
+  par.outE  = (float*)d_out;
+  par.outN  = (float*)d_out + NE*5;
+
+  static int grid_sz = 0;
+  if (grid_sz == 0) {
+    int nb = 0;
+    hipOccupancyMaxActiveBlocksPerMultiprocessor(&nb, k_all, 256, 0);
+    int dev = 0;
+    hipGetDevice(&dev);
+    hipDeviceProp_t prop;
+    hipGetDeviceProperties(&prop, dev);
+    int g = nb * prop.multiProcessorCount;
+    if (g > MAXGRID) g = MAXGRID;
+    if (g < 32) g = 32;
+    grid_sz = g;
+  }
+  void* args[] = { (void*)&par };
+  hipLaunchCooperativeKernel((void*)k_all, dim3(grid_sz), dim3(256), args, 0, stream);
+}
```

New measurement: 474.1 us. +178.8%, slower.
